# Kernel tuning notes

Hardware: AMD Instinct MI355X
Metric: run time of the kernel (lower is better)

## Reference

```python
import jax, jax.numpy as jnp
import numpy as np

N_USER = 100000
M_ITEM = 50000
N_NODE = N_USER + M_ITEM
D = 64           # latent_dim
WD = D // 2      # word_emb_dim
FU = FI = 10     # padded feature-bag width
NUF = NIF = 30000
VOCAB = 20000
T = 8            # tokens per text source (name/comment/comment_list)
DNU = DNI = 10   # numeric feature dims
B = 2048         # seed batch
S = 20           # sampled neighbors per layer
L = 2            # num_layers


def setup_inputs() -> dict:
    key = jax.random.key(0)
    ks = jax.random.split(key, 26)
    f = lambda i, s: jax.random.normal(ks[i], s, jnp.float32) * 0.05
    ri = lambda i, s, hi: jax.random.randint(ks[i], s, 0, hi)
    return {
        # int (graph / lookup) inputs
        "seeds": ri(0, (B,), N_USER),
        "neigh1": ri(1, (B, S), N_NODE),
        "neigh2": ri(2, (B, S, S), N_NODE),
        "user_feat_idx": ri(3, (N_USER, FU), NUF),
        "item_feat_idx": ri(4, (M_ITEM, FI), NIF),
        "user_text_idx": ri(5, (N_USER, 3, T), VOCAB),
        "item_text_idx": ri(6, (M_ITEM, 3, T), VOCAB),
        # float tables / features
        "user_id_emb": f(7, (N_USER, D)),
        "item_id_emb": f(8, (M_ITEM, D)),
        "user_feat_emb": f(9, (NUF, D)),
        "item_feat_emb": f(10, (NIF, D)),
        "word_emb": f(11, (VOCAB, WD)),
        "user_word300": f(12, (N_USER, 300)),
        "item_word300": f(13, (M_ITEM, 300)),
        "item_sent768": f(14, (M_ITEM, 768)),
        "user_numeric": f(15, (N_USER, DNU)),
        "item_numeric": f(16, (M_ITEM, DNI)),
        # linears (stored as (in, out); y = x @ W + b)
        "Wnum_u": f(17, (DNU, D)), "bnum_u": jnp.zeros((D,), jnp.float32),
        "Wnum_i": f(18, (DNI, D)), "bnum_i": jnp.zeros((D,), jnp.float32),
        "Wproj_u": f(19, (int(D * 3.5) + 300, D)), "bproj_u": jnp.zeros((D,), jnp.float32),
        "Wproj_i": f(20, (int(D * 3.5) + 300 + 768, D)), "bproj_i": jnp.zeros((D,), jnp.float32),
        "W_w": f(21, (L, 2 * D, D)), "b_w": jnp.zeros((L, D), jnp.float32),
        "W_v": f(22, (L, D, D)), "b_v": jnp.zeros((L, D), jnp.float32),
    }


def _forward(user_id_emb, item_id_emb, user_feat_emb, item_feat_emb, word_emb,
             user_word300, item_word300, item_sent768, user_numeric, item_numeric,
             Wnum_u, bnum_u, Wnum_i, bnum_i, Wproj_u, bproj_u, Wproj_i, bproj_i,
             W_w, b_w, W_v, b_v,
             seeds, neigh1, neigh2, user_feat_idx, item_feat_idx,
             user_text_idx, item_text_idx):
    # --- multi-source node embeddings (get_text_embedding + proj + numeric) ---
    # text: mean-pool word embeddings per source, concat 3 sources -> 1.5*D
    u_text = word_emb[user_text_idx].mean(axis=2).reshape(N_USER, 3 * WD)
    i_text = word_emb[item_text_idx].mean(axis=2).reshape(M_ITEM, 3 * WD)
    # feature bags: mean-pooled embedding lookup
    u_feat = user_feat_emb[user_feat_idx].mean(axis=1)
    i_feat = item_feat_emb[item_feat_idx].mean(axis=1)
    u = (jnp.concatenate([user_id_emb, u_feat, u_text, user_word300], -1) @ Wproj_u
         + bproj_u + user_numeric @ Wnum_u + bnum_u)
    it = (jnp.concatenate([item_id_emb, i_feat, i_text, item_word300, item_sent768], -1) @ Wproj_i
          + bproj_i + item_numeric @ Wnum_i + bnum_i)
    x = jnp.concatenate([u, it], axis=0)  # [N_NODE, D], items offset by N_USER

    # --- neighbor-sampled GraphSAGE: h = W_l([self, mean(V_l(neigh))]) ---
    def sage(l, self_x, neigh_x, act):
        agg = (neigh_x @ W_v[l] + b_v[l]).mean(axis=-2)
        h = jnp.concatenate([self_x, agg], axis=-1) @ W_w[l] + b_w[l]
        return jax.nn.relu(h) if act else h

    x0 = x[seeds]        # [B, D]
    x1 = x[neigh1]       # [B, S, D]
    x2 = x[neigh2]       # [B, S, S, D]
    h1 = sage(0, x1, x2, True)   # layer-0 applied to 1-hop nodes
    h0 = sage(0, x0, x1, True)   # layer-0 applied to seeds
    out = sage(1, h0, h1, False)  # final layer, no activation
    return out  # [B, D]


def reference(seeds, neigh1, neigh2, user_feat_idx, item_feat_idx, user_text_idx,
              item_text_idx, user_id_emb, item_id_emb, user_feat_emb, item_feat_emb,
              word_emb, user_word300, item_word300, item_sent768, user_numeric,
              item_numeric, Wnum_u, bnum_u, Wnum_i, bnum_i, Wproj_u, bproj_u,
              Wproj_i, bproj_i, W_w, b_w, W_v, b_v):
    return _forward(user_id_emb, item_id_emb, user_feat_emb, item_feat_emb, word_emb,
                    user_word300, item_word300, item_sent768, user_numeric, item_numeric,
                    Wnum_u, bnum_u, Wnum_i, bnum_i, Wproj_u, bproj_u, Wproj_i, bproj_i,
                    W_w, b_w, W_v, b_v,
                    seeds, neigh1, neigh2, user_feat_idx, item_feat_idx,
                    user_text_idx, item_text_idx)
```

## Files before the change

### kernel.cpp

```cpp
#include <hip/hip_runtime.h>
#include <hip/hip_bf16.h>
#include <stdint.h>

#define N_USER 100000
#define M_ITEM 50000
#define N_NODE 150000
#define B_SEED 2048
#define S_NB 20
#define UBLK2 1563
#define IBLK2 782
#define DEPTH 4

typedef __bf16   bf16x8 __attribute__((ext_vector_type(8)));
typedef float    f32x4  __attribute__((ext_vector_type(4)));
typedef uint32_t u32x4  __attribute__((ext_vector_type(4)));

typedef __attribute__((address_space(3))) uint32_t lds_u32_t;
typedef __attribute__((address_space(1))) const uint32_t glb_u32_t;

__device__ __forceinline__ uint16_t f2bf(float f) {
    uint32_t u = __float_as_uint(f);
    return (uint16_t)((u + 0x7FFFu + ((u >> 16) & 1u)) >> 16);
}
__device__ __forceinline__ uint32_t pk2(float a, float b) {
    __hip_bfloat162 h = __float22bfloat162_rn(make_float2(a, b));
    return *reinterpret_cast<uint32_t*>(&h);
}
__device__ __forceinline__ float bf2f(uint16_t u) {
    return __uint_as_float(((uint32_t)u) << 16);
}

union BF8 { bf16x8 v; uint32_t u[4]; };

__device__ __forceinline__ bf16x8 pack8v(f32x4 lo, f32x4 hi) {
    BF8 r;
    r.u[0] = pk2(lo[0], lo[1]); r.u[1] = pk2(lo[2], lo[3]);
    r.u[2] = pk2(hi[0], hi[1]); r.u[3] = pk2(hi[2], hi[3]);
    return r.v;
}
__device__ __forceinline__ bf16x8 ldf32x8_mask(const float* rowp, int base, int limit) {
    BF8 r;
#pragma unroll
    for (int h = 0; h < 4; ++h) {
        const int k0 = base + 2 * h;
        const float a = (k0     < limit) ? rowp[k0]     : 0.f;
        const float b = (k0 + 1 < limit) ? rowp[k0 + 1] : 0.f;
        r.u[h] = pk2(a, b);
    }
    return r.v;
}

template<int N> __device__ __forceinline__ void waitcnt_vm() {
    asm volatile("s_waitcnt vmcnt(%0)" :: "n"(N) : "memory");
    __builtin_amdgcn_sched_barrier(0);
}

__global__ void prep_kernel(const float* __restrict__ Wproj_u, const float* __restrict__ Wnum_u,
                            const float* __restrict__ Wproj_i, const float* __restrict__ Wnum_i,
                            const float* __restrict__ Wv0, const float* __restrict__ Ww0,
                            uint16_t* __restrict__ WTU, uint16_t* __restrict__ WTI,
                            uint16_t* __restrict__ WvT, uint16_t* __restrict__ WwT)
{
    const int idx = blockIdx.x * 256 + threadIdx.x;
    if (idx < 36864) {
        const int d = idx / 576, kp = idx - d * 576;
        float v = 0.f;
        if (kp < 160)      v = Wproj_u[(64 + kp) * 64 + d];
        else if (kp < 192) { const int j = kp - 160; if (j < 10) v = Wnum_u[j * 64 + d]; }
        else if (kp < 224) { const int j = kp - 192; if (j < 12) v = Wproj_u[(512 + j) * 64 + d]; }
        else if (kp < 288) v = Wproj_u[(kp - 224) * 64 + d];
        else               v = Wproj_u[(224 + kp - 288) * 64 + d];
        WTU[d * 576 + kp] = f2bf(v);
    } else if (idx < 122880) {
        const int i2 = idx - 36864;
        const int d = i2 / 1344, kp = i2 - d * 1344;
        float v = 0.f;
        if (kp < 160)      v = Wproj_i[(64 + kp) * 64 + d];
        else if (kp < 192) { const int j = kp - 160; if (j < 10) v = Wnum_i[j * 64 + d]; }
        else if (kp < 224) { const int j = kp - 192; if (j < 12) v = Wproj_i[(512 + j) * 64 + d]; }
        else if (kp < 288) v = Wproj_i[(kp - 224) * 64 + d];
        else if (kp < 576) v = Wproj_i[(224 + kp - 288) * 64 + d];
        else               v = Wproj_i[(524 + kp - 576) * 64 + d];
        WTI[d * 1344 + kp] = f2bf(v);
    } else {
        const int i2 = idx - 122880;
        if (i2 < 4096) { const int d = i2 >> 6, k = i2 & 63;  WvT[d * 64 + k]  = f2bf(Wv0[k * 64 + d]); }
        else           { const int j = i2 - 4096;
                         const int d = j >> 7, k = j & 127;   WwT[d * 128 + k] = f2bf(Ww0[k * 64 + d]); }
    }
}

__global__ __launch_bounds__(256) void gpack_kernel(
    const int* __restrict__ ufi, const int* __restrict__ ifi,
    const int* __restrict__ uti, const int* __restrict__ iti,
    const float* __restrict__ ufe, const float* __restrict__ ife,
    const float* __restrict__ wemb,
    uint16_t* __restrict__ Apre)
{
    const int gid  = blockIdx.x * 256 + threadIdx.x;
    const int node = gid >> 3;
    const int d0   = gid & 7;
    if (node >= N_NODE) return;
    const bool item = node >= N_USER;
    const int nloc  = item ? node - N_USER : node;
    const int*   fidx = (item ? ifi : ufi) + (size_t)nloc * 10;
    const int*   tidx = (item ? iti : uti) + (size_t)nloc * 24;
    const float* fe   = item ? ife : ufe;
    uint16_t* out = Apre + (size_t)node * 160;

    {
        f32x4 s0 = {0, 0, 0, 0}, s1 = {0, 0, 0, 0};
#pragma unroll
        for (int j = 0; j < 10; ++j) {
            const float* p = fe + (size_t)fidx[j] * 64 + 8 * d0;
            s0 += *(const f32x4*)p;
            s1 += *(const f32x4*)(p + 4);
        }
        s0 *= 0.1f; s1 *= 0.1f;
        uint4 o = make_uint4(pk2(s0[0], s0[1]), pk2(s0[2], s0[3]),
                             pk2(s1[0], s1[1]), pk2(s1[2], s1[3]));
        *(uint4*)(out + 8 * d0) = o;
    }
#pragma unroll
    for (int s = 0; s < 3; ++s) {
        f32x4 a = {0, 0, 0, 0};
#pragma unroll
        for (int j = 0; j < 8; ++j) {
            const float* p = wemb + (size_t)tidx[s * 8 + j] * 32 + 4 * d0;
            a += *(const f32x4*)p;
        }
        a *= 0.125f;
        *(uint2*)(out + 64 + 32 * s + 4 * d0) = make_uint2(pk2(a[0], a[1]), pk2(a[2], a[3]));
    }
}

__global__ __launch_bounds__(256) void pgemm_kernel(
    const uint16_t* __restrict__ Apre,
    const float* __restrict__ u_id,  const float* __restrict__ i_id,
    const float* __restrict__ uw300, const float* __restrict__ iw300,
    const float* __restrict__ is768,
    const float* __restrict__ unum,  const float* __restrict__ inum,
    const uint16_t* __restrict__ WTU, const uint16_t* __restrict__ WTI,
    const float* __restrict__ bproj_u, const float* __restrict__ bnum_u,
    const float* __restrict__ bproj_i, const float* __restrict__ bnum_i,
    uint16_t* __restrict__ xout)
{
    __shared__ float buf[DEPTH][2048];

    const int t = threadIdx.x;
    const int w = t >> 6, l = t & 63;
    const int l15 = l & 15, g4 = l >> 4;
    const bool item = blockIdx.x < IBLK2;
    const int tile  = item ? blockIdx.x : (blockIdx.x - IBLK2);
    const int ntype = item ? M_ITEM : N_USER;
    const int nb    = tile * 64;
    const int NC    = item ? 35 : 11;

    const float* idp = item ? i_id  : u_id;
    const float* w3p = item ? iw300 : uw300;
    const float* nmp = item ? inum  : unum;
    const uint16_t* WT = item ? WTI : WTU;
    const int KP       = item ? 1344 : 576;

    f32x4 acc[4] = {};
    const uint16_t* WTb = WT + (size_t)l15 * KP + g4 * 8;

    auto MM = [&](bf16x8 af, int kb) {
#pragma unroll
        for (int db = 0; db < 4; ++db) {
            const bf16x8 bfr = *reinterpret_cast<const bf16x8*>(WTb + (size_t)db * 16 * KP + kb);
            acc[db] = __builtin_amdgcn_mfma_f32_16x16x32_bf16(af, bfr, acc[db], 0, 0, 0);
        }
    };

    auto stage = [&](int bi, int c) {
        const float* base; int stride, coloff;
        if (c < 2)       { base = idp;    stride = 64;  coloff = c * 32; }
        else if (c < 11) { base = w3p;    stride = 300; coloff = (c - 2) * 32; }
        else             { base = is768;  stride = 768; coloff = (c - 11) * 32; }
#pragma unroll
        for (int j = 0; j < 2; ++j) {
            const int row  = w * 16 + j * 8 + (l >> 3);
            const int node = (nb + row) < ntype ? (nb + row) : (ntype - 1);
            const int swb  = ((l & 7) * 16) ^ ((row & 7) << 4);
            const float* g = base + (size_t)node * stride + coloff + (swb >> 2);
            uint32_t* lp = (uint32_t*)((char*)&buf[bi][0] + w * 2048 + j * 1024);
            __builtin_amdgcn_global_load_lds((glb_u32_t*)g, (lds_u32_t*)lp, 16, 0, 0);
        }
    };

    auto compute = [&](int bi, int kb) {
        const char* bb = (const char*)&buf[bi][0];
        const int r = w * 16 + l15;
        const f32x4 lo = *(const f32x4*)(bb + r * 128 + ((g4 * 32)      ^ ((r & 7) << 4)));
        const f32x4 hi = *(const f32x4*)(bb + r * 128 + ((g4 * 32 + 16) ^ ((r & 7) << 4)));
        MM(pack8v(lo, hi), kb);
    };

    const int nloc = (nb + w * 16 + l15) < ntype ? (nb + w * 16 + l15) : (ntype - 1);
    const int node = (item ? N_USER : 0) + nloc;
    const uint16_t* ap = Apre + (size_t)node * 160 + g4 * 8;
    bf16x8 af[5];
#pragma unroll
    for (int ks = 0; ks < 5; ++ks) af[ks] = *(const bf16x8*)(ap + ks * 32);
    const bf16x8 numf  = ldf32x8_mask(nmp + (size_t)nloc * 10, g4 * 8, 10);
    const bf16x8 tailf = ldf32x8_mask(w3p + (size_t)nloc * 300, 288 + g4 * 8, 300);

#pragma unroll
    for (int d = 0; d < DEPTH - 1; ++d) stage(d, d);

#pragma unroll
    for (int ks = 0; ks < 5; ++ks) MM(af[ks], ks * 32);
    MM(numf, 160);
    MM(tailf, 192);

#pragma unroll 1
    for (int c = 0; c < NC - (DEPTH - 1); ++c) {
        stage((c + DEPTH - 1) & (DEPTH - 1), c + DEPTH - 1);
        waitcnt_vm<2 * (DEPTH - 1)>();
        compute(c & (DEPTH - 1), 224 + 32 * c);
    }
    waitcnt_vm<4>(); compute((NC - 3) & (DEPTH - 1), 224 + 32 * (NC - 3));
    waitcnt_vm<2>(); compute((NC - 2) & (DEPTH - 1), 224 + 32 * (NC - 2));
    waitcnt_vm<0>(); compute((NC - 1) & (DEPTH - 1), 224 + 32 * (NC - 1));

    const int nb_out = nb + w * 16 + g4 * 4;
    const float* bp = item ? bproj_i : bproj_u;
    const float* bn = item ? bnum_i  : bnum_u;
    uint16_t* xo = xout + (size_t)(item ? N_USER : 0) * 64;
#pragma unroll
    for (int db = 0; db < 4; ++db) {
        const int d = db * 16 + l15;
        const float bias = bp[d] + bn[d];
#pragma unroll
        for (int r = 0; r < 4; ++r) {
            const int nn = nb_out + r;
            if (nn < ntype) xo[(size_t)nn * 64 + d] = f2bf(acc[db][r] + bias);
        }
    }
}

__global__ __launch_bounds__(256) void xv_kernel(
    const uint16_t* __restrict__ x, const uint16_t* __restrict__ WvT,
    const float* __restrict__ bv, uint16_t* __restrict__ xv, int n)
{
    const int t = threadIdx.x;
    const int w = t >> 6, l = t & 63, l15 = l & 15, g4 = l >> 4;
    const int node = blockIdx.x * 64 + w * 16 + l15;
    const int node_c = node < n ? node : n - 1;

    f32x4 acc[4] = {};
    const uint16_t* WTb = WvT + l15 * 64 + g4 * 8;
#pragma unroll
    for (int ks = 0; ks < 2; ++ks) {
        const bf16x8 af = *reinterpret_cast<const bf16x8*>(x + (size_t)node_c * 64 + ks * 32 + g4 * 8);
#pragma unroll
        for (int db = 0; db < 4; ++db) {
            const bf16x8 bfr = *reinterpret_cast<const bf16x8*>(WTb + db * 16 * 64 + ks * 32);
            acc[db] = __builtin_amdgcn_mfma_f32_16x16x32_bf16(af, bfr, acc[db], 0, 0, 0);
        }
    }
    const int node_base = blockIdx.x * 64 + w * 16 + g4 * 4;
#pragma unroll
    for (int db = 0; db < 4; ++db) {
        const int d = db * 16 + l15;
        const float bias = bv[d];
#pragma unroll
        for (int r = 0; r < 4; ++r) {
            const int nn = node_base + r;
            if (nn < n) xv[(size_t)nn * 64 + d] = f2bf(acc[db][r] + bias);
        }
    }
}

__global__ __launch_bounds__(256) void sage_mfma_kernel(
    const uint16_t* __restrict__ x, const uint16_t* __restrict__ xv,
    const int* __restrict__ self_idx, const int* __restrict__ neigh_idx,
    const uint16_t* __restrict__ WwT, const float* __restrict__ bw,
    uint16_t* __restrict__ out, int relu)
{
    const int t = threadIdx.x;
    const int w = t >> 6, l = t & 63, l15 = l & 15, g4 = l >> 4;
    const int r = blockIdx.x * 64 + w * 16 + l15;
    const int sidx = self_idx[r];
    const int* ni = neigh_idx + (size_t)r * S_NB;

    f32x4 acc[4] = {};
    const uint16_t* WTb = WwT + l15 * 128 + g4 * 8;

    auto MM = [&](bf16x8 af, int kb) {
#pragma unroll
        for (int db = 0; db < 4; ++db) {
            const bf16x8 bfr = *reinterpret_cast<const bf16x8*>(WTb + db * 16 * 128 + kb);
            acc[db] = __builtin_amdgcn_mfma_f32_16x16x32_bf16(af, bfr, acc[db], 0, 0, 0);
        }
    };

#pragma unroll
    for (int ks = 0; ks < 2; ++ks) {
        const bf16x8 af = *reinterpret_cast<const bf16x8*>(x + (size_t)sidx * 64 + ks * 32 + g4 * 8);
        MM(af, ks * 32);
    }
#pragma unroll
    for (int ks = 0; ks < 2; ++ks) {
        float ev[4] = {0.f, 0.f, 0.f, 0.f}, od[4] = {0.f, 0.f, 0.f, 0.f};
#pragma unroll
        for (int j = 0; j < S_NB; ++j) {
            const u32x4 v = *reinterpret_cast<const u32x4*>(xv + (size_t)ni[j] * 64 + ks * 32 + g4 * 8);
#pragma unroll
            for (int q = 0; q < 4; ++q) {
                ev[q] += __uint_as_float(v[q] << 16);
                od[q] += __uint_as_float(v[q] & 0xffff0000u);
            }
        }
        BF8 m;
#pragma unroll
        for (int q = 0; q < 4; ++q) m.u[q] = pk2(ev[q] * (1.f / S_NB), od[q] * (1.f / S_NB));
        MM(m.v, 64 + ks * 32);
    }

    const int rb = blockIdx.x * 64 + w * 16 + g4 * 4;
#pragma unroll
    for (int db = 0; db < 4; ++db) {
        const int d = db * 16 + l15;
        const float bias = bw[d];
#pragma unroll
        for (int rr = 0; rr < 4; ++rr) {
            float h = acc[db][rr] + bias;
            if (relu) h = fmaxf(h, 0.f);
            out[(size_t)(rb + rr) * 64 + d] = f2bf(h);
        }
    }
}

__global__ __launch_bounds__(256) void final_kernel(
    const uint16_t* __restrict__ h0, const uint16_t* __restrict__ h1,
    const float* __restrict__ Wv, const float* __restrict__ bv,
    const float* __restrict__ Ww, const float* __restrict__ bw,
    float* __restrict__ out)
{
    __shared__ float WvL[64 * 64];
    __shared__ float WwL[128 * 64];
    const int t = threadIdx.x;
    for (int i = t; i < 64 * 64; i += 256)  WvL[i] = Wv[i];
    for (int i = t; i < 128 * 64; i += 256) WwL[i] = Ww[i];
    __syncthreads();

    const int wave = t >> 6, lane = t & 63;
    const int base = blockIdx.x * 32 + wave * 8;
    const float bvl = bv[lane], bwl = bw[lane];

    for (int i = 0; i < 8; ++i) {
        const int b = base + i;
        float m = 0.f;
#pragma unroll
        for (int s = 0; s < S_NB; ++s)
            m += bf2f(h1[(size_t)(b * S_NB + s) * 64 + lane]);
        m *= (1.f / S_NB);

        float agg = bvl;
#pragma unroll 8
        for (int k = 0; k < 64; ++k)
            agg += __shfl(m, k) * WvL[k * 64 + lane];

        const float selfv = bf2f(h0[(size_t)b * 64 + lane]);
        float h = bwl;
#pragma unroll 8
        for (int k = 0; k < 64; ++k)
            h += __shfl(selfv, k) * WwL[k * 64 + lane];
#pragma unroll 8
        for (int k = 0; k < 64; ++k)
            h += __shfl(agg, k) * WwL[(64 + k) * 64 + lane];

        out[(size_t)b * 64 + lane] = h;
    }
}

extern "C" void kernel_launch(void* const* d_in, const int* in_sizes, int n_in,
                              void* d_out, int out_size, void* d_ws, size_t ws_size,
                              hipStream_t stream)
{
    const int*   seeds   = (const int*)d_in[0];
    const int*   neigh1  = (const int*)d_in[1];
    const int*   neigh2  = (const int*)d_in[2];
    const int*   ufi     = (const int*)d_in[3];
    const int*   ifi     = (const int*)d_in[4];
    const int*   uti     = (const int*)d_in[5];
    const int*   iti     = (const int*)d_in[6];
    const float* u_id    = (const float*)d_in[7];
    const float* i_id    = (const float*)d_in[8];
    const float* ufe     = (const float*)d_in[9];
    const float* ife     = (const float*)d_in[10];
    const float* wemb    = (const float*)d_in[11];
    const float* uw300   = (const float*)d_in[12];
    const float* iw300   = (const float*)d_in[13];
    const float* is768   = (const float*)d_in[14];
    const float* unum    = (const float*)d_in[15];
    const float* inum    = (const float*)d_in[16];
    const float* Wnum_u  = (const float*)d_in[17];
    const float* bnum_u  = (const float*)d_in[18];
    const float* Wnum_i  = (const float*)d_in[19];
    const float* bnum_i  = (const float*)d_in[20];
    const float* Wproj_u = (const float*)d_in[21];
    const float* bproj_u = (const float*)d_in[22];
    const float* Wproj_i = (const float*)d_in[23];
    const float* bproj_i = (const float*)d_in[24];
    const float* W_w     = (const float*)d_in[25];
    const float* b_w     = (const float*)d_in[26];
    const float* W_v     = (const float*)d_in[27];
    const float* b_v     = (const float*)d_in[28];

    uint16_t* WTU  = (uint16_t*)d_ws;
    uint16_t* WTI  = WTU  + 36864;
    uint16_t* WvT0 = WTI  + 86016;
    uint16_t* WwT0 = WvT0 + 4096;
    uint16_t* xbf  = WwT0 + 8192;
    uint16_t* xvbf = xbf  + (size_t)N_NODE * 64;
    uint16_t* h1bf = xvbf + (size_t)N_NODE * 64;
    uint16_t* h0bf = h1bf + (size_t)B_SEED * S_NB * 64;
    uint16_t* Apre = xvbf;
    float* outp = (float*)d_out;

    prep_kernel<<<528, 256, 0, stream>>>(
        Wproj_u, Wnum_u, Wproj_i, Wnum_i, W_v, W_w, WTU, WTI, WvT0, WwT0);

    gpack_kernel<<<(N_NODE * 8 + 255) / 256, 256, 0, stream>>>(
        ufi, ifi, uti, iti, ufe, ife, wemb, Apre);

    pgemm_kernel<<<UBLK2 + IBLK2, 256, 0, stream>>>(
        Apre, u_id, i_id, uw300, iw300, is768, unum, inum,
        WTU, WTI, bproj_u, bnum_u, bproj_i, bnum_i, xbf);

    xv_kernel<<<(N_NODE + 63) / 64, 256, 0, stream>>>(xbf, WvT0, b_v, xvbf, N_NODE);

    sage_mfma_kernel<<<(B_SEED * S_NB) / 64, 256, 0, stream>>>(
        xbf, xvbf, neigh1, neigh2, WwT0, b_w, h1bf, 1);
    sage_mfma_kernel<<<B_SEED / 64, 256, 0, stream>>>(
        xbf, xvbf, seeds, neigh1, WwT0, b_w, h0bf, 1);

    final_kernel<<<B_SEED / 32, 256, 0, stream>>>(
        h0bf, h1bf, W_v + 4096, b_v + 64, W_w + 8192, b_w + 64, outp);
}
```

Before: 353.0 us.

## Stage weight fragments via async LDS loads alongside activations, double-buffered

The projection GEMM now fetches weight B-fragments for the streamed chunks asynchronously into LDS with global_load_lds, together with the activation tiles, instead of loading them synchronously from global memory right before each MFMA. To make room in LDS, the pipeline depth drops from four buffers to a per-wave double buffer. This aims to hide weight-load latency, but the shallower prefetch may leave activation gather latency less hidden, and LDS per block grows.

```diff
diff --git a/kernel.cpp b/kernel.cpp
--- a/kernel.cpp
+++ b/kernel.cpp
@@ -9,7 +9,6 @@
 #define S_NB 20
 #define UBLK2 1563
 #define IBLK2 782
-#define DEPTH 4
 
 typedef __bf16   bf16x8 __attribute__((ext_vector_type(8)));
 typedef float    f32x4  __attribute__((ext_vector_type(4)));
@@ -145,7 +144,7 @@
     const float* __restrict__ bproj_i, const float* __restrict__ bnum_i,
     uint16_t* __restrict__ xout)
 {
-    __shared__ float buf[DEPTH][2048];
+    __shared__ char lds[2][4][6144];
 
     const int t = threadIdx.x;
     const int w = t >> 6, l = t & 63;
@@ -173,28 +172,44 @@
         }
     };
 
+    const uint16_t* WTfrag = WT + (size_t)l15 * KP + g4 * 8;
+
     auto stage = [&](int bi, int c) {
         const float* base; int stride, coloff;
         if (c < 2)       { base = idp;    stride = 64;  coloff = c * 32; }
         else if (c < 11) { base = w3p;    stride = 300; coloff = (c - 2) * 32; }
         else             { base = is768;  stride = 768; coloff = (c - 11) * 32; }
+        char* wbase = &lds[bi][w][0];
 #pragma unroll
         for (int j = 0; j < 2; ++j) {
-            const int row  = w * 16 + j * 8 + (l >> 3);
-            const int node = (nb + row) < ntype ? (nb + row) : (ntype - 1);
-            const int swb  = ((l & 7) * 16) ^ ((row & 7) << 4);
+            const int rl   = j * 8 + (l >> 3);
+            const int nn   = nb + w * 16 + rl;
+            const int node = nn < ntype ? nn : (ntype - 1);
+            const int swb  = ((l & 7) * 16) ^ ((rl & 7) << 4);
             const float* g = base + (size_t)node * stride + coloff + (swb >> 2);
-            uint32_t* lp = (uint32_t*)((char*)&buf[bi][0] + w * 2048 + j * 1024);
-            __builtin_amdgcn_global_load_lds((glb_u32_t*)g, (lds_u32_t*)lp, 16, 0, 0);
+            __builtin_amdgcn_global_load_lds((glb_u32_t*)g,
+                (lds_u32_t*)(void*)(wbase + j * 1024), 16, 0, 0);
+        }
+        const int kb = 224 + 32 * c;
+#pragma unroll
+        for (int i = 0; i < 4; ++i) {
+            const uint16_t* g = WTfrag + (size_t)i * 16 * KP + kb;
+            __builtin_amdgcn_global_load_lds((glb_u32_t*)g,
+                (lds_u32_t*)(void*)(wbase + 2048 + i * 1024), 16, 0, 0);
         }
     };
 
-    auto compute = [&](int bi, int kb) {
-        const char* bb = (const char*)&buf[bi][0];
-        const int r = w * 16 + l15;
-        const f32x4 lo = *(const f32x4*)(bb + r * 128 + ((g4 * 32)      ^ ((r & 7) << 4)));
-        const f32x4 hi = *(const f32x4*)(bb + r * 128 + ((g4 * 32 + 16) ^ ((r & 7) << 4)));
-        MM(pack8v(lo, hi), kb);
+    auto compute = [&](int bi) {
+        const char* wbase = &lds[bi][w][0];
+        const int r = l15;
+        const f32x4 lo = *(const f32x4*)(wbase + r * 128 + ((g4 * 32)      ^ ((r & 7) << 4)));
+        const f32x4 hi = *(const f32x4*)(wbase + r * 128 + ((g4 * 32 + 16) ^ ((r & 7) << 4)));
+        const bf16x8 af = pack8v(lo, hi);
+#pragma unroll
+        for (int db = 0; db < 4; ++db) {
+            const bf16x8 bfr = *(const bf16x8*)(wbase + 2048 + db * 1024 + l * 16);
+            acc[db] = __builtin_amdgcn_mfma_f32_16x16x32_bf16(af, bfr, acc[db], 0, 0, 0);
+        }
     };
 
     const int nloc = (nb + w * 16 + l15) < ntype ? (nb + w * 16 + l15) : (ntype - 1);
@@ -206,23 +221,20 @@
     const bf16x8 numf  = ldf32x8_mask(nmp + (size_t)nloc * 10, g4 * 8, 10);
     const bf16x8 tailf = ldf32x8_mask(w3p + (size_t)nloc * 300, 288 + g4 * 8, 300);
 
-#pragma unroll
-    for (int d = 0; d < DEPTH - 1; ++d) stage(d, d);
-
+    stage(0, 0);
 #pragma unroll
     for (int ks = 0; ks < 5; ++ks) MM(af[ks], ks * 32);
     MM(numf, 160);
     MM(tailf, 192);
 
 #pragma unroll 1
-    for (int c = 0; c < NC - (DEPTH - 1); ++c) {
-        stage((c + DEPTH - 1) & (DEPTH - 1), c + DEPTH - 1);
-        waitcnt_vm<2 * (DEPTH - 1)>();
-        compute(c & (DEPTH - 1), 224 + 32 * c);
-    }
-    waitcnt_vm<4>(); compute((NC - 3) & (DEPTH - 1), 224 + 32 * (NC - 3));
-    waitcnt_vm<2>(); compute((NC - 2) & (DEPTH - 1), 224 + 32 * (NC - 2));
-    waitcnt_vm<0>(); compute((NC - 1) & (DEPTH - 1), 224 + 32 * (NC - 1));
+    for (int c = 0; c < NC - 1; ++c) {
+        stage((c + 1) & 1, c + 1);
+        waitcnt_vm<6>();
+        compute(c & 1);
+    }
+    waitcnt_vm<0>();
+    compute((NC - 1) & 1);
 
     const int nb_out = nb + w * 16 + g4 * 4;
     const float* bp = item ? bproj_i : bproj_u;
```

Measured after the change: 347.4 us. Within noise of the previous version (-1.6%).
